# Kernel tuning notes

Hardware: AMD Instinct MI355X
Metric: run time of the kernel (lower is better)

## Reference

```python
import jax, jax.numpy as jnp
import numpy as np

LAMBDA = 20.0   # lambda_val (blackbox-diff smoothing)
REG = 0.5       # reg
MAX_LABEL = 8   # labels drawn in [0, MAX_LABEL)


def _pairwise_dist(x):
    # x: [n, d] -> [n, n] euclidean distances (safe sqrt, exact 0 on diagonal)
    sq = jnp.sum(x * x, axis=-1)
    d2 = sq[:, None] + sq[None, :] - 2.0 * (x @ x.T)
    d2 = jnp.maximum(d2, 0.0)
    return jnp.where(d2 > 0, jnp.sqrt(jnp.where(d2 > 0, d2, 1.0)), 0.0)


def _single_linkage_adj(D, k):
    # Agglomerative (single-linkage) clustering of n points given [n,n] dists,
    # stopped at k clusters; returns [n,n] 0/1 cluster-adjacency matrix.
    n = D.shape[0]
    BIG = jnp.asarray(1e9, D.dtype)
    eye = jnp.eye(n, dtype=bool)
    Dw0 = jnp.where(eye, BIG, D)
    labels0 = jnp.arange(n)
    active0 = jnp.ones((n,), dtype=bool)

    def step(carry, _):
        Dw, labels, active = carry
        mask = active[:, None] & active[None, :] & ~eye
        flat = jnp.argmin(jnp.where(mask, Dw, BIG))
        i, j = flat // n, flat % n
        a = jnp.minimum(i, j)
        b = jnp.maximum(i, j)
        newrow = jnp.minimum(Dw[a], Dw[b])        # single linkage merge
        Dw = Dw.at[a, :].set(newrow).at[:, a].set(newrow)
        active = active.at[b].set(False)
        labels = jnp.where(labels == b, a, labels)
        return (Dw, labels, active), labels

    _, hist = jax.lax.scan(step, (Dw0, labels0, active0), None, length=n - 1)
    all_hist = jnp.concatenate([labels0[None, :], hist], axis=0)  # [n, n]; row m = labels after m merges (n-m clusters)
    lab = all_hist[n - k]
    return (lab[:, None] == lab[None, :]).astype(D.dtype)


def _solve(dists, ks):
    return jax.vmap(_single_linkage_adj)(dists, ks)


def setup_inputs() -> dict:
    key = jax.random.key(0)
    k1, k2, k3 = jax.random.split(key, 3)
    B, n, d = 256, 64, 768
    return {
        "query_embedding": jax.random.normal(k1, (B, d), dtype=jnp.float32),
        "psg_embeddings": jax.random.normal(k2, (B, n, d), dtype=jnp.float32),
        "labels": jax.random.randint(k3, (B, n), 0, MAX_LABEL, dtype=jnp.int64)
        if jax.config.jax_enable_x64 else jax.random.randint(k3, (B, n), 0, MAX_LABEL, dtype=jnp.int32),
    }


def reference(query_embedding, psg_embeddings, labels):
    # true_adj_mat: adj[i,j] = 1 iff i==j or label[i]==label[j] (diag is label-equal anyway)
    true_adj = (labels[:, :, None] == labels[:, None, :]).astype(jnp.float32)  # [B,n,n]
    # ks[i] = number of unique labels in sample i
    presence = (labels[..., None] == jnp.arange(MAX_LABEL)).any(axis=1)  # [B, MAX_LABEL]
    ks = presence.sum(axis=-1)

    scaled = query_embedding[:, None, :] * psg_embeddings            # [B,n,d]
    dists = jax.vmap(_pairwise_dist)(scaled)                          # [B,n,n]

    mean_similar = (dists * true_adj).sum() / true_adj.sum()
    mean_dissimilar = (dists * (1.0 - true_adj)).sum() / (1.0 - true_adj).sum()

    adj = _solve(dists, ks)                                           # OptimCluster forward
    err = adj * (1.0 - true_adj) + (1.0 - adj) * true_adj
    err_mean = err.mean(axis=0).sum()
    return err_mean + REG * (mean_similar - mean_dissimilar)
```

## Files before the change

kernel.cpp:

```cpp
#include <hip/hip_runtime.h>


#define NPTS 64
#define DIM 768
#define CH 128
#define NCH 6
#define NT 512
#define BIGF 1e9f
#define PGS 68

typedef __attribute__((ext_vector_type(8))) __bf16 bf16x8;
typedef __attribute__((ext_vector_type(4))) float f32x4;
typedef __attribute__((ext_vector_type(8))) unsigned short us8;

__device__ __forceinline__ void lds_fence() {
  asm volatile("s_waitcnt lgkmcnt(0)" ::: "memory");
  __builtin_amdgcn_sched_barrier(0);
}

__device__ __forceinline__ void split3(float x, unsigned short& h,
                                       unsigned short& m, unsigned short& l) {
  unsigned u = __float_as_uint(x);
  unsigned rb = (u + 0x7FFFu + ((u >> 16) & 1u)) & 0xFFFF0000u;
  h = (unsigned short)(rb >> 16);
  float r1 = x - __uint_as_float(rb);
  unsigned u1 = __float_as_uint(r1);
  unsigned rb1 = (u1 + 0x7FFFu + ((u1 >> 16) & 1u)) & 0xFFFF0000u;
  m = (unsigned short)(rb1 >> 16);
  float r2 = r1 - __uint_as_float(rb1);
  l = (unsigned short)(__float_as_uint(r2) >> 16);
}

__global__ __launch_bounds__(NT) void fused_kernel(
    const float* __restrict__ q,
    const float* __restrict__ psg,
    const int*   __restrict__ labels,
    float* __restrict__ simS_o, float* __restrict__ disS_o,
    int* __restrict__ simC_o, int* __restrict__ errC_o)
{
  __shared__ __align__(16) unsigned short Hml[2][3][NPTS][CH];
  __shared__ __align__(16) float PG[NPTS * PGS];
  __shared__ float diagf[NPTS];
  __shared__ __align__(16) int cls[NPTS];
  __shared__ __align__(16) int comp_s[NPTS];
  __shared__ unsigned bw_s[NPTS], bfl_s[NPTS];
  __shared__ int ptr_s[NPTS], lab_s[NPTS];
  __shared__ __align__(8) unsigned long long ekey_s[NPTS];
  __shared__ int ecnt_s;

  const int b = blockIdx.x;
  const int t = threadIdx.x;
  const int w = t >> 6;
  const int l = t & 63;

  const float* qb = q + (size_t)b * DIM;
  const float* pb = psg + (size_t)b * NPTS * DIM;

  const int row0 = t >> 4;
  const int gran = t & 15;
  const float* pr0 = pb + (size_t)row0 * DIM + (gran << 3);
  const float* pr1 = pr0 + 32 * DIM;
  const float* qr  = qb + (gran << 3);

  const int rw = w >> 1;
  const int R = rw >> 1, C = rw & 1;
  const int ksub = w & 1;
  const int lrow = l & 15;

  f32x4 acc[2][2];
  {
    f32x4 z = {0.f, 0.f, 0.f, 0.f};
    acc[0][0] = z; acc[0][1] = z; acc[1][0] = z; acc[1][1] = z;
  }

  float4 pva[2][2], qv[2];
  pva[0][0] = *(const float4*)(pr0 + 0);
  pva[0][1] = *(const float4*)(pr0 + 4);
  pva[1][0] = *(const float4*)(pr1 + 0);
  pva[1][1] = *(const float4*)(pr1 + 4);
  qv[0] = *(const float4*)(qr + 0);
  qv[1] = *(const float4*)(qr + 4);

  #pragma unroll
  for (int rr = 0; rr < 2; ++rr) {
    const int row = row0 + (rr << 5);
    float xs[8];
    xs[0] = pva[rr][0].x * qv[0].x; xs[1] = pva[rr][0].y * qv[0].y;
    xs[2] = pva[rr][0].z * qv[0].z; xs[3] = pva[rr][0].w * qv[0].w;
    xs[4] = pva[rr][1].x * qv[1].x; xs[5] = pva[rr][1].y * qv[1].y;
    xs[6] = pva[rr][1].z * qv[1].z; xs[7] = pva[rr][1].w * qv[1].w;
    us8 uh, um, ul;
    #pragma unroll
    for (int e = 0; e < 8; ++e) {
      unsigned short hh, mm, ll;
      split3(xs[e], hh, mm, ll);
      uh[e] = hh; um[e] = mm; ul[e] = ll;
    }
    const int p = gran ^ (row & 15);
    *reinterpret_cast<us8*>(&Hml[0][0][row][p << 3]) = uh;
    *reinterpret_cast<us8*>(&Hml[0][1][row][p << 3]) = um;
    *reinterpret_cast<us8*>(&Hml[0][2][row][p << 3]) = ul;
  }
  __syncthreads();

  #pragma unroll 1
  for (int c = 0; c < NCH; ++c) {
    const int cur = c & 1;
    if (c + 1 < NCH) {
      const int off = (c + 1) * CH;
      pva[0][0] = *(const float4*)(pr0 + off);
      pva[0][1] = *(const float4*)(pr0 + off + 4);
      pva[1][0] = *(const float4*)(pr1 + off);
      pva[1][1] = *(const float4*)(pr1 + off + 4);
      qv[0] = *(const float4*)(qr + off);
      qv[1] = *(const float4*)(qr + off + 4);
    }

    #pragma unroll 1
    for (int ss = 0; ss < 2; ++ss) {
      const int s = ksub + (ss << 1);
      const int p = ((s << 2) + (l >> 4)) ^ lrow;
      bf16x8 fa[3][2], fb[3][2];
      #pragma unroll
      for (int v = 0; v < 3; ++v)
        #pragma unroll
        for (int tb = 0; tb < 2; ++tb) {
          const int row = (R << 5) + (tb << 4) + lrow;
          fa[v][tb] = *reinterpret_cast<const bf16x8*>(&Hml[cur][v][row][p << 3]);
        }
      if (R != C) {
        #pragma unroll
        for (int v = 0; v < 3; ++v)
          #pragma unroll
          for (int tb = 0; tb < 2; ++tb) {
            const int row = (C << 5) + (tb << 4) + lrow;
            fb[v][tb] = *reinterpret_cast<const bf16x8*>(&Hml[cur][v][row][p << 3]);
          }
      } else {
        #pragma unroll
        for (int v = 0; v < 3; ++v)
          #pragma unroll
          for (int tb = 0; tb < 2; ++tb) fb[v][tb] = fa[v][tb];
      }
      #pragma unroll
      for (int ti = 0; ti < 2; ++ti)
        #pragma unroll
        for (int tj = 0; tj < 2; ++tj) {
          acc[ti][tj] = __builtin_amdgcn_mfma_f32_16x16x32_bf16(fa[0][ti], fb[0][tj], acc[ti][tj], 0, 0, 0);
          acc[ti][tj] = __builtin_amdgcn_mfma_f32_16x16x32_bf16(fa[0][ti], fb[1][tj], acc[ti][tj], 0, 0, 0);
          acc[ti][tj] = __builtin_amdgcn_mfma_f32_16x16x32_bf16(fa[1][ti], fb[0][tj], acc[ti][tj], 0, 0, 0);
          acc[ti][tj] = __builtin_amdgcn_mfma_f32_16x16x32_bf16(fa[1][ti], fb[1][tj], acc[ti][tj], 0, 0, 0);
          acc[ti][tj] = __builtin_amdgcn_mfma_f32_16x16x32_bf16(fa[0][ti], fb[2][tj], acc[ti][tj], 0, 0, 0);
          acc[ti][tj] = __builtin_amdgcn_mfma_f32_16x16x32_bf16(fa[2][ti], fb[0][tj], acc[ti][tj], 0, 0, 0);
        }
    }

    if (c + 1 < NCH) {
      #pragma unroll
      for (int rr = 0; rr < 2; ++rr) {
        const int row = row0 + (rr << 5);
        float xs[8];
        xs[0] = pva[rr][0].x * qv[0].x; xs[1] = pva[rr][0].y * qv[0].y;
        xs[2] = pva[rr][0].z * qv[0].z; xs[3] = pva[rr][0].w * qv[0].w;
        xs[4] = pva[rr][1].x * qv[1].x; xs[5] = pva[rr][1].y * qv[1].y;
        xs[6] = pva[rr][1].z * qv[1].z; xs[7] = pva[rr][1].w * qv[1].w;
        us8 uh, um, ul;
        #pragma unroll
        for (int e = 0; e < 8; ++e) {
          unsigned short hh, mm, ll;
          split3(xs[e], hh, mm, ll);
          uh[e] = hh; um[e] = mm; ul[e] = ll;
        }
        const int p = gran ^ (row & 15);
        *reinterpret_cast<us8*>(&Hml[cur ^ 1][0][row][p << 3]) = uh;
        *reinterpret_cast<us8*>(&Hml[cur ^ 1][1][row][p << 3]) = um;
        *reinterpret_cast<us8*>(&Hml[cur ^ 1][2][row][p << 3]) = ul;
      }
    }
    __syncthreads();
  }

  if (w & 1) {
    float* dst = PG + (rw << 10);
    #pragma unroll
    for (int ti = 0; ti < 2; ++ti)
      #pragma unroll
      for (int tj = 0; tj < 2; ++tj)
        *reinterpret_cast<f32x4*>(dst + (((ti << 1) + tj) << 8) + (l << 2)) = acc[ti][tj];
  }
  __syncthreads();
  if (!(w & 1)) {
    const float* src = PG + (rw << 10);
    #pragma unroll
    for (int ti = 0; ti < 2; ++ti)
      #pragma unroll
      for (int tj = 0; tj < 2; ++tj)
        acc[ti][tj] += *reinterpret_cast<const f32x4*>(src + (((ti << 1) + tj) << 8) + (l << 2));
  }
  __syncthreads();
  if (!(w & 1)) {
    #pragma unroll
    for (int ti = 0; ti < 2; ++ti)
      #pragma unroll
      for (int tj = 0; tj < 2; ++tj)
        #pragma unroll
        for (int reg = 0; reg < 4; ++reg) {
          const int grow = (R << 5) + (ti << 4) + ((l >> 4) << 2) + reg;
          const int gcol = (C << 5) + (tj << 4) + (l & 15);
          PG[grow * PGS + gcol] = acc[ti][tj][reg];
        }
  }
  __syncthreads();

  if (t < NPTS) diagf[t] = PG[t * PGS + t];
  __syncthreads();
  {
    const int r  = t >> 3;
    const int c0 = (t & 7) << 3;
    const float dr = diagf[r];
    #pragma unroll
    for (int e = 0; e < 8; ++e) {
      const int cc = c0 + e;
      const float gg = PG[r * PGS + cc];
      float d2 = dr + diagf[cc] - 2.f * gg;
      d2 = fmaxf(d2, 0.f);
      PG[r * PGS + cc] = (d2 > 0.f) ? sqrtf(d2) : 0.f;
    }
  }
  __syncthreads();
  if (w != 0) return;

  float drow[64];
  #pragma unroll
  for (int v4 = 0; v4 < 16; ++v4) {
    f32x4 x = *reinterpret_cast<const f32x4*>(&PG[l * PGS + (v4 << 2)]);
    drow[v4 * 4 + 0] = x[0]; drow[v4 * 4 + 1] = x[1];
    drow[v4 * 4 + 2] = x[2]; drow[v4 * 4 + 3] = x[3];
  }
  int tl = labels[b * NPTS + l];

  unsigned long long sMask = 0ull;
  int kcnt = 0;
  #pragma unroll
  for (int v = 0; v < 8; ++v) {
    unsigned long long mv = __ballot(tl == v);
    kcnt += (mv != 0ull) ? 1 : 0;
    if (tl == v) sMask = mv;
  }
  int simC = __popcll(sMask);
  const int merges = NPTS - kcnt;

  float simS = 0.f, disS = 0.f;
  #pragma unroll
  for (int j = 0; j < NPTS; ++j) {
    bool sim = (sMask >> j) & 1ull;
    simS += sim ? drow[j] : 0.f;
    disS += sim ? 0.f : drow[j];
  }

  comp_s[l] = l; lab_s[l] = l;
  if (l == 0) ecnt_s = 0;
  lds_fence();

  #pragma unroll 1
  for (int rd = 0; rd < 6; ++rd) {
    bw_s[l] = 0xFFFFFFFFu; bfl_s[l] = 0xFFFFFFFFu;
    lds_fence();
    const int myc = comp_s[l];
    float bv = BIGF; int bj = 64;
    #pragma unroll
    for (int jc = 0; jc < 16; ++jc) {
      int4 c4 = *reinterpret_cast<const int4*>(&comp_s[jc << 2]);
      int cj[4] = {c4.x, c4.y, c4.z, c4.w};
      #pragma unroll
      for (int e = 0; e < 4; ++e) {
        const int j = (jc << 2) + e;
        bool ok = (cj[e] != myc) && (drow[j] < bv);
        bv = ok ? drow[j] : bv;
        bj = ok ? j : bj;
      }
    }
    if (bj < 64) atomicMin(&bw_s[myc], __float_as_uint(bv));
    lds_fence();
    unsigned bwc = bw_s[myc];
    if (bj < 64 && __float_as_uint(bv) == bwc)
      atomicMin(&bfl_s[myc], (unsigned)((l << 6) | bj));
    lds_fence();
    const bool isroot = (myc == l);
    const unsigned rw_ = bw_s[l];
    const unsigned rf  = bfl_s[l];
    int hook = l;
    if (isroot && rw_ != 0xFFFFFFFFu)
      hook = comp_s[rf & 63];
    ptr_s[l] = isroot ? hook : myc;
    lds_fence();
    if (isroot && hook != l) {
      const int pd = ptr_s[hook];
      if (pd == l && l < hook) {
        ptr_s[l] = l;
      } else {
        int slot = atomicAdd(&ecnt_s, 1);
        ekey_s[slot & 63] = ((unsigned long long)rw_ << 32) | (unsigned long long)rf;
      }
    }
    lds_fence();
    #pragma unroll 1
    for (int jj = 0; jj < 6; ++jj) {
      int pp = ptr_s[l];
      int p2 = ptr_s[pp & 63];
      ptr_s[l] = p2;
    }
    lds_fence();
    comp_s[l] = ptr_s[l];
    lds_fence();
  }

  const int ec = ecnt_s;
  const bool ehave = (l < ec);
  const unsigned long long my = ehave ? ekey_s[l] : ~0ull;
  int rank = 0;
  #pragma unroll 7
  for (int j = 0; j < 63; ++j) {
    unsigned long long kj = ekey_s[j];
    rank += (j < ec && kj < my) ? 1 : 0;
  }
  const bool kept = ehave && (rank < merges);
  const int eu = (int)((my >> 6) & 63);
  const int ev = (int)(my & 63);

  #pragma unroll 1
  for (int iter = 0; iter < 64; ++iter) {
    int m = 0; bool ch = false;
    if (kept) {
      int lu = lab_s[eu], lv = lab_s[ev];
      m = min(lu, lv);
      ch = (m < lu) || (m < lv);
    }
    if (__ballot(ch) == 0ull) break;
    if (ch) {
      atomicMin(&lab_s[eu], m);
      atomicMin(&lab_s[ev], m);
    }
    lds_fence();
  }
  lds_fence();
  const int cl = lab_s[l];

  cls[l] = cl;
  lds_fence();
  unsigned long long cMask = 0ull;
  const int4* cp = reinterpret_cast<const int4*>(cls);
  #pragma unroll 4
  for (int jq = 0; jq < 16; ++jq) {
    int4 c4 = cp[jq];
    cMask |= ((unsigned long long)(c4.x == cl)) << (jq * 4 + 0);
    cMask |= ((unsigned long long)(c4.y == cl)) << (jq * 4 + 1);
    cMask |= ((unsigned long long)(c4.z == cl)) << (jq * 4 + 2);
    cMask |= ((unsigned long long)(c4.w == cl)) << (jq * 4 + 3);
  }
  int ec2 = __popcll(cMask ^ sMask);

  #pragma unroll
  for (int off = 32; off; off >>= 1) {
    simS += __shfl_xor(simS, off);
    disS += __shfl_xor(disS, off);
    simC += __shfl_xor(simC, off);
    ec2  += __shfl_xor(ec2, off);
  }
  if (l == 0) {
    simS_o[b] = simS; disS_o[b] = disS;
    simC_o[b] = simC; errC_o[b] = ec2;
  }
}

__global__ __launch_bounds__(64) void finalize_kernel(
    const float* __restrict__ simS, const float* __restrict__ disS,
    const int* __restrict__ simC, const int* __restrict__ errC,
    float* __restrict__ out)
{
  const int l = threadIdx.x;
  double ss = 0.0, dd = 0.0, sc = 0.0, ec = 0.0;
  #pragma unroll
  for (int r = 0; r < 4; ++r) {
    int i = (r << 6) + l;
    ss += (double)simS[i];
    dd += (double)disS[i];
    sc += (double)simC[i];
    ec += (double)errC[i];
  }
  #pragma unroll
  for (int off = 32; off; off >>= 1) {
    ss += __shfl_xor(ss, off);
    dd += __shfl_xor(dd, off);
    sc += __shfl_xor(sc, off);
    ec += __shfl_xor(ec, off);
  }
  if (l == 0) {
    const double total = 256.0 * 4096.0;
    double ms = ss / sc;
    double md = dd / (total - sc);
    out[0] = (float)(ec / 256.0 + 0.5 * (ms - md));
  }
}

extern "C" void kernel_launch(void* const* d_in, const int* in_sizes, int n_in,
                              void* d_out, int out_size, void* d_ws, size_t ws_size,
                              hipStream_t stream) {
  const float* q      = (const float*)d_in[0];
  const float* psg    = (const float*)d_in[1];
  const int*   labels = (const int*)d_in[2];
  float* out = (float*)d_out;

  float* simS = (float*)d_ws;
  float* disS = simS + 256;
  int*   simC = (int*)(disS + 256);
  int*   errC = simC + 256;

  fused_kernel<<<256, NT, 0, stream>>>(q, psg, labels, simS, disS, simC, errC);
  finalize_kernel<<<1, 64, 0, stream>>>(simS, disS, simC, errC, out);
}
```

Baseline: 36.53 us.

## Prefetch global loads two chunks ahead and add early exits to component loops

```diff
diff --git a/kernel.cpp b/kernel.cpp
--- a/kernel.cpp
+++ b/kernel.cpp
@@ -30,6 +30,88 @@
   float r2 = r1 - __uint_as_float(rb1);
   l = (unsigned short)(__float_as_uint(r2) >> 16);
 }
+
+__device__ __forceinline__ void stage_chunk(
+    unsigned short (*Hb)[NPTS][CH], const float4 (&pva)[2][2],
+    const float4 (&qv)[2], int row0, int gran) {
+  #pragma unroll
+  for (int rr = 0; rr < 2; ++rr) {
+    const int row = row0 + (rr << 5);
+    float xs[8];
+    xs[0] = pva[rr][0].x * qv[0].x; xs[1] = pva[rr][0].y * qv[0].y;
+    xs[2] = pva[rr][0].z * qv[0].z; xs[3] = pva[rr][0].w * qv[0].w;
+    xs[4] = pva[rr][1].x * qv[1].x; xs[5] = pva[rr][1].y * qv[1].y;
+    xs[6] = pva[rr][1].z * qv[1].z; xs[7] = pva[rr][1].w * qv[1].w;
+    us8 uh, um, ul;
+    #pragma unroll
+    for (int e = 0; e < 8; ++e) {
+      unsigned short hh, mm, ll;
+      split3(xs[e], hh, mm, ll);
+      uh[e] = hh; um[e] = mm; ul[e] = ll;
+    }
+    const int p = gran ^ (row & 15);
+    *reinterpret_cast<us8*>(&Hb[0][row][p << 3]) = uh;
+    *reinterpret_cast<us8*>(&Hb[1][row][p << 3]) = um;
+    *reinterpret_cast<us8*>(&Hb[2][row][p << 3]) = ul;
+  }
+}
+
+__device__ __forceinline__ void mfma_chunk(
+    const unsigned short (*Hb)[NPTS][CH], f32x4 (&acc)[2][2],
+    int R, int C, int ksub, int lrow, int lhi) {
+  #pragma unroll 1
+  for (int ss = 0; ss < 2; ++ss) {
+    const int s = ksub + (ss << 1);
+    const int p = ((s << 2) + lhi) ^ lrow;
+    bf16x8 fa[3][2], fb[3][2];
+    #pragma unroll
+    for (int v = 0; v < 3; ++v)
+      #pragma unroll
+      for (int tb = 0; tb < 2; ++tb) {
+        const int row = (R << 5) + (tb << 4) + lrow;
+        fa[v][tb] = *reinterpret_cast<const bf16x8*>(&Hb[v][row][p << 3]);
+      }
+    if (R != C) {
+      #pragma unroll
+      for (int v = 0; v < 3; ++v)
+        #pragma unroll
+        for (int tb = 0; tb < 2; ++tb) {
+          const int row = (C << 5) + (tb << 4) + lrow;
+          fb[v][tb] = *reinterpret_cast<const bf16x8*>(&Hb[v][row][p << 3]);
+        }
+    } else {
+      #pragma unroll
+      for (int v = 0; v < 3; ++v)
+        #pragma unroll
+        for (int tb = 0; tb < 2; ++tb) fb[v][tb] = fa[v][tb];
+    }
+    #pragma unroll
+    for (int ti = 0; ti < 2; ++ti)
+      #pragma unroll
+      for (int tj = 0; tj < 2; ++tj) {
+        acc[ti][tj] = __builtin_amdgcn_mfma_f32_16x16x32_bf16(fa[0][ti], fb[0][tj], acc[ti][tj], 0, 0, 0);
+        acc[ti][tj] = __builtin_amdgcn_mfma_f32_16x16x32_bf16(fa[0][ti], fb[1][tj], acc[ti][tj], 0, 0, 0);
+        acc[ti][tj] = __builtin_amdgcn_mfma_f32_16x16x32_bf16(fa[1][ti], fb[0][tj], acc[ti][tj], 0, 0, 0);
+        acc[ti][tj] = __builtin_amdgcn_mfma_f32_16x16x32_bf16(fa[1][ti], fb[1][tj], acc[ti][tj], 0, 0, 0);
+        acc[ti][tj] = __builtin_amdgcn_mfma_f32_16x16x32_bf16(fa[0][ti], fb[2][tj], acc[ti][tj], 0, 0, 0);
+        acc[ti][tj] = __builtin_amdgcn_mfma_f32_16x16x32_bf16(fa[2][ti], fb[0][tj], acc[ti][tj], 0, 0, 0);
+      }
+  }
+}
+
+#define ISSUE_P(PV, cix) do {                                       \
+    const int off_ = (cix) * CH;                                    \
+    PV[0][0] = *(const float4*)(pr0 + off_);                        \
+    PV[0][1] = *(const float4*)(pr0 + off_ + 4);                    \
+    PV[1][0] = *(const float4*)(pr1 + off_);                        \
+    PV[1][1] = *(const float4*)(pr1 + off_ + 4);                    \
+  } while (0)
+
+#define ISSUE_Q(QV, cix) do {                                       \
+    const int off_ = (cix) * CH;                                    \
+    QV[0] = *(const float4*)(qr + off_);                            \
+    QV[1] = *(const float4*)(qr + off_ + 4);                        \
+  } while (0)
 
 __global__ __launch_bounds__(NT) void fused_kernel(
     const float* __restrict__ q,
@@ -66,6 +148,7 @@
   const int R = rw >> 1, C = rw & 1;
   const int ksub = w & 1;
   const int lrow = l & 15;
+  const int lhi  = l >> 4;
 
   f32x4 acc[2][2];
   {
@@ -73,110 +156,27 @@
     acc[0][0] = z; acc[0][1] = z; acc[1][0] = z; acc[1][1] = z;
   }
 
-  float4 pva[2][2], qv[2];
-  pva[0][0] = *(const float4*)(pr0 + 0);
-  pva[0][1] = *(const float4*)(pr0 + 4);
-  pva[1][0] = *(const float4*)(pr1 + 0);
-  pva[1][1] = *(const float4*)(pr1 + 4);
-  qv[0] = *(const float4*)(qr + 0);
-  qv[1] = *(const float4*)(qr + 4);
-
-  #pragma unroll
-  for (int rr = 0; rr < 2; ++rr) {
-    const int row = row0 + (rr << 5);
-    float xs[8];
-    xs[0] = pva[rr][0].x * qv[0].x; xs[1] = pva[rr][0].y * qv[0].y;
-    xs[2] = pva[rr][0].z * qv[0].z; xs[3] = pva[rr][0].w * qv[0].w;
-    xs[4] = pva[rr][1].x * qv[1].x; xs[5] = pva[rr][1].y * qv[1].y;
-    xs[6] = pva[rr][1].z * qv[1].z; xs[7] = pva[rr][1].w * qv[1].w;
-    us8 uh, um, ul;
-    #pragma unroll
-    for (int e = 0; e < 8; ++e) {
-      unsigned short hh, mm, ll;
-      split3(xs[e], hh, mm, ll);
-      uh[e] = hh; um[e] = mm; ul[e] = ll;
-    }
-    const int p = gran ^ (row & 15);
-    *reinterpret_cast<us8*>(&Hml[0][0][row][p << 3]) = uh;
-    *reinterpret_cast<us8*>(&Hml[0][1][row][p << 3]) = um;
-    *reinterpret_cast<us8*>(&Hml[0][2][row][p << 3]) = ul;
-  }
+  float4 pvaA[2][2], pvaB[2][2], qv[2];
+
+  ISSUE_P(pvaA, 0);
+  ISSUE_Q(qv, 0);
+  ISSUE_P(pvaB, 1);
+  stage_chunk(Hml[0], pvaA, qv, row0, gran);
   __syncthreads();
 
   #pragma unroll 1
-  for (int c = 0; c < NCH; ++c) {
-    const int cur = c & 1;
-    if (c + 1 < NCH) {
-      const int off = (c + 1) * CH;
-      pva[0][0] = *(const float4*)(pr0 + off);
-      pva[0][1] = *(const float4*)(pr0 + off + 4);
-      pva[1][0] = *(const float4*)(pr1 + off);
-      pva[1][1] = *(const float4*)(pr1 + off + 4);
-      qv[0] = *(const float4*)(qr + off);
-      qv[1] = *(const float4*)(qr + off + 4);
-    }
-
-    #pragma unroll 1
-    for (int ss = 0; ss < 2; ++ss) {
-      const int s = ksub + (ss << 1);
-      const int p = ((s << 2) + (l >> 4)) ^ lrow;
-      bf16x8 fa[3][2], fb[3][2];
-      #pragma unroll
-      for (int v = 0; v < 3; ++v)
-        #pragma unroll
-        for (int tb = 0; tb < 2; ++tb) {
-          const int row = (R << 5) + (tb << 4) + lrow;
-          fa[v][tb] = *reinterpret_cast<const bf16x8*>(&Hml[cur][v][row][p << 3]);
-        }
-      if (R != C) {
-        #pragma unroll
-        for (int v = 0; v < 3; ++v)
-          #pragma unroll
-          for (int tb = 0; tb < 2; ++tb) {
-            const int row = (C << 5) + (tb << 4) + lrow;
-            fb[v][tb] = *reinterpret_cast<const bf16x8*>(&Hml[cur][v][row][p << 3]);
-          }
-      } else {
-        #pragma unroll
-        for (int v = 0; v < 3; ++v)
-          #pragma unroll
-          for (int tb = 0; tb < 2; ++tb) fb[v][tb] = fa[v][tb];
-      }
-      #pragma unroll
-      for (int ti = 0; ti < 2; ++ti)
-        #pragma unroll
-        for (int tj = 0; tj < 2; ++tj) {
-          acc[ti][tj] = __builtin_amdgcn_mfma_f32_16x16x32_bf16(fa[0][ti], fb[0][tj], acc[ti][tj], 0, 0, 0);
-          acc[ti][tj] = __builtin_amdgcn_mfma_f32_16x16x32_bf16(fa[0][ti], fb[1][tj], acc[ti][tj], 0, 0, 0);
-          acc[ti][tj] = __builtin_amdgcn_mfma_f32_16x16x32_bf16(fa[1][ti], fb[0][tj], acc[ti][tj], 0, 0, 0);
-          acc[ti][tj] = __builtin_amdgcn_mfma_f32_16x16x32_bf16(fa[1][ti], fb[1][tj], acc[ti][tj], 0, 0, 0);
-          acc[ti][tj] = __builtin_amdgcn_mfma_f32_16x16x32_bf16(fa[0][ti], fb[2][tj], acc[ti][tj], 0, 0, 0);
-          acc[ti][tj] = __builtin_amdgcn_mfma_f32_16x16x32_bf16(fa[2][ti], fb[0][tj], acc[ti][tj], 0, 0, 0);
-        }
-    }
-
-    if (c + 1 < NCH) {
-      #pragma unroll
-      for (int rr = 0; rr < 2; ++rr) {
-        const int row = row0 + (rr << 5);
-        float xs[8];
-        xs[0] = pva[rr][0].x * qv[0].x; xs[1] = pva[rr][0].y * qv[0].y;
-        xs[2] = pva[rr][0].z * qv[0].z; xs[3] = pva[rr][0].w * qv[0].w;
-        xs[4] = pva[rr][1].x * qv[1].x; xs[5] = pva[rr][1].y * qv[1].y;
-        xs[6] = pva[rr][1].z * qv[1].z; xs[7] = pva[rr][1].w * qv[1].w;
-        us8 uh, um, ul;
-        #pragma unroll
-        for (int e = 0; e < 8; ++e) {
-          unsigned short hh, mm, ll;
-          split3(xs[e], hh, mm, ll);
-          uh[e] = hh; um[e] = mm; ul[e] = ll;
-        }
-        const int p = gran ^ (row & 15);
-        *reinterpret_cast<us8*>(&Hml[cur ^ 1][0][row][p << 3]) = uh;
-        *reinterpret_cast<us8*>(&Hml[cur ^ 1][1][row][p << 3]) = um;
-        *reinterpret_cast<us8*>(&Hml[cur ^ 1][2][row][p << 3]) = ul;
-      }
-    }
+  for (int cc = 0; cc < 3; ++cc) {
+    if (cc < 2) ISSUE_P(pvaA, 2 * cc + 2);
+    ISSUE_Q(qv, 2 * cc + 1);
+    mfma_chunk(Hml[0], acc, R, C, ksub, lrow, lhi);
+    stage_chunk(Hml[1], pvaB, qv, row0, gran);
+    __syncthreads();
+    if (cc < 2) {
+      ISSUE_P(pvaB, 2 * cc + 3);
+      ISSUE_Q(qv, 2 * cc + 2);
+    }
+    mfma_chunk(Hml[1], acc, R, C, ksub, lrow, lhi);
+    if (cc < 2) stage_chunk(Hml[0], pvaA, qv, row0, gran);
     __syncthreads();
   }
 
@@ -205,8 +205,8 @@
       for (int tj = 0; tj < 2; ++tj)
         #pragma unroll
         for (int reg = 0; reg < 4; ++reg) {
-          const int grow = (R << 5) + (ti << 4) + ((l >> 4) << 2) + reg;
-          const int gcol = (C << 5) + (tj << 4) + (l & 15);
+          const int grow = (R << 5) + (ti << 4) + (lhi << 2) + reg;
+          const int gcol = (C << 5) + (tj << 4) + lrow;
           PG[grow * PGS + gcol] = acc[ti][tj][reg];
         }
   }
@@ -308,11 +308,15 @@
     for (int jj = 0; jj < 6; ++jj) {
       int pp = ptr_s[l];
       int p2 = ptr_s[pp & 63];
+      if (__ballot(p2 != pp) == 0ull) break;
       ptr_s[l] = p2;
     }
     lds_fence();
-    comp_s[l] = ptr_s[l];
-    lds_fence();
+    const int newc = ptr_s[l];
+    comp_s[l] = newc;
+    lds_fence();
+    const int base = __shfl(newc, 0);
+    if (__ballot(newc != base) == 0ull) break;
   }
 
   const int ec = ecnt_s;
```

After: 32.41 us. -11.3%, faster.
